# Performance work log

Hardware: AMD Instinct MI355X
Metric: run time of the kernel (lower is better)

Reference implementation:

```python
import jax, jax.numpy as jnp
import numpy as np

B, P, T, H, M = 32, 64, 256, 128, 16
MEAS_E, MOT_E = 64, 64
E = MEAS_E + MOT_E  # total_emb = 128
MAP_SIZE, MAP_EMB = 18, 128
ALPHA = 0.5  # soft-resampling alpha
OUT_DIM = 32 * 9 * 9  # encode output: conv1 stride2 18->9, conv2/3 stride1


def setup_inputs() -> dict:
    key = jax.random.key(0)
    ks = jax.random.split(key, 24)
    def g(i, shape, scale=0.05):
        return jax.random.normal(ks[i], shape, dtype=jnp.float32) * scale
    return {
        "map_in": jax.random.normal(ks[0], (B, 1, MAP_SIZE, MAP_SIZE), dtype=jnp.float32),
        "measurement_in": jax.random.normal(ks[1], (B, T, M), dtype=jnp.float32),
        "motion_in": jax.random.normal(ks[2], (B, T, 3), dtype=jnp.float32),
        "h0": jax.random.uniform(ks[3], (B * P, H), dtype=jnp.float32),
        "eps": jax.random.normal(ks[4], (T, B * P, H), dtype=jnp.float32),
        "u": jax.random.uniform(ks[5], (T, B, P), dtype=jnp.float32),
        "conv1_w": g(6, (16, 1, 5, 5)),
        "conv2_w": g(7, (32, 16, 3, 3)),
        "conv3_w": g(8, (32, 32, 3, 3)),
        "W_mapemb": g(9, (OUT_DIM, MAP_EMB)), "b_mapemb": jnp.zeros((MAP_EMB,), jnp.float32),
        "W_m2meas": g(10, (MAP_EMB, MEAS_E)), "b_m2meas": jnp.zeros((MEAS_E,), jnp.float32),
        "W_m2mot": g(11, (MAP_EMB, MOT_E)), "b_m2mot": jnp.zeros((MOT_E,), jnp.float32),
        "W_meas": g(12, (M, MEAS_E)), "b_meas": jnp.zeros((MEAS_E,), jnp.float32),
        "W_mot": g(13, (3, MOT_E)), "b_mot": jnp.zeros((MOT_E,), jnp.float32),
        "Wz": g(14, (H + E, H)), "bz": jnp.zeros((H,), jnp.float32),
        "Wr": g(15, (H + E, H)), "br": jnp.zeros((H,), jnp.float32),
        "Wn": g(16, (H + E, 2 * H)), "bn": jnp.zeros((2 * H,), jnp.float32),
        "Wo": g(17, (H + E, 1)), "bo": jnp.zeros((1,), jnp.float32),
        "W_label": g(18, (H, 3)), "b_label": jnp.zeros((3,), jnp.float32),
    }


def _encode(map_in, c1, c2, c3):
    # Conv -> ReLU -> BatchNorm(eval: identity w/ default stats) -> Dropout(eval: identity)
    dn = ("NCHW", "OIHW", "NCHW")
    x = jax.lax.conv_general_dilated(map_in, c1, (2, 2), [(2, 2), (2, 2)], dimension_numbers=dn)
    x = jax.nn.relu(x)
    x = jax.lax.conv_general_dilated(x, c2, (1, 1), [(1, 1), (1, 1)], dimension_numbers=dn)
    x = jax.nn.relu(x)
    x = jax.lax.conv_general_dilated(x, c3, (1, 1), [(1, 1), (1, 1)], dimension_numbers=dn)
    return jax.nn.relu(x)


def _pf_forward(map_in, measurement_in, motion_in, h0, eps, u,
                conv1_w, conv2_w, conv3_w,
                W_mapemb, b_mapemb, W_m2meas, b_m2meas, W_m2mot, b_m2mot,
                W_meas, b_meas, W_mot, b_mot,
                Wz, bz, Wr, br, Wn, bn, Wo, bo, W_label, b_label):
    relu = jax.nn.relu
    emb_map = _encode(map_in, conv1_w, conv2_w, conv3_w).reshape(B, -1)
    emb_map = relu(emb_map @ W_mapemb + b_mapemb)
    meas_map = relu(emb_map @ W_m2meas + b_m2meas)           # [B, MEAS_E]
    mot_map = relu(emb_map @ W_m2mot + b_m2mot)              # [B, MOT_E]
    emb_meas = relu(measurement_in @ W_meas + b_meas)        # [B, T, MEAS_E]
    emb_mot = relu(motion_in @ W_mot + b_mot)                # [B, T, MOT_E]
    embedding = jnp.concatenate([emb_meas * meas_map[:, None, :],
                                 emb_mot * mot_map[:, None, :]], axis=2)  # [B,T,E]
    embedding = jnp.tile(embedding, (P, 1, 1))               # [P*B, T, E] (repeat(pNumber,1,1))
    xs_emb = jnp.swapaxes(embedding, 0, 1)                   # [T, P*B, E]
    p0 = jnp.full((B * P, 1), np.log(1.0 / P), dtype=jnp.float32)
    inv_p = (1.0 - ALPHA) / P

    def cell(carry, step):
        h, p = carry                                         # [PB,H], [PB,1]
        x, ep, uu = step                                     # [PB,E], [PB,H], [B,P]
        hx = jnp.concatenate([h, x], axis=1)
        z = jax.nn.sigmoid(hx @ Wz + bz)
        r = jax.nn.sigmoid(hx @ Wr + br)
        n = jnp.concatenate([r * h, x], axis=1) @ Wn + bn
        mu, var = jnp.split(n, 2, axis=1)
        n = mu + ep * jax.nn.softplus(var)                   # reparameterize
        h1 = (1.0 - z) * n + z * h
        lp = jnp.concatenate([h1, x], axis=1) @ Wo + bo + p  # [PB,1] log obs-likelihood + prior
        lp = jax.nn.log_softmax(lp.reshape(P, B), axis=0)    # normalize over particles
        # soft resampling: q = alpha*w + (1-alpha)/P, inverse-CDF multinomial
        w = ALPHA * jnp.exp(lp) + inv_p                      # [P,B], sums to 1 over P
        cdf = jnp.cumsum(w.T, axis=1)                        # [B,P]
        idx = jax.vmap(lambda c, uv: jnp.searchsorted(c, uv * c[-1]))(cdf, uu)
        idx = jnp.clip(idx, 0, P - 1)                        # [B,P]
        idxT = idx.T                                         # [P,B]
        h_new = jnp.take_along_axis(h1.reshape(P, B, H), idxT[:, :, None], axis=0)
        p_g = jnp.take_along_axis(jnp.exp(lp), idxT, axis=0) # [P,B]
        p_new = jnp.log(ALPHA * p_g + inv_p)
        p_new = p_new - jax.scipy.special.logsumexp(p_new, axis=0, keepdims=True)
        h_new = h_new.reshape(B * P, H)
        p_new = p_new.reshape(B * P, 1)
        return (h_new, p_new), (h_new, p_new)

    _, (hs, ps) = jax.lax.scan(cell, (h0, p0), (xs_emb, eps, u))
    # hs: [T, PB, H]; hnn_dropout in eval mode -> identity
    y = jnp.sum(hs.reshape(T, P, B, H) * jnp.exp(ps.reshape(T, P, B, 1)), axis=1)  # [T,B,H]
    y_out = jax.nn.sigmoid(y @ W_label + b_label)            # sigmoid(xy)+sigmoid(h) == sigmoid(all)
    pf_out = jax.nn.sigmoid(hs @ W_label + b_label)          # [T, PB, 3]
    return y_out, pf_out


def reference(map_in, measurement_in, motion_in, h0, eps, u,
              conv1_w, conv2_w, conv3_w,
              W_mapemb, b_mapemb, W_m2meas, b_m2meas, W_m2mot, b_m2mot,
              W_meas, b_meas, W_mot, b_mot,
              Wz, bz, Wr, br, Wn, bn, Wo, bo, W_label, b_label):
    return _pf_forward(map_in, measurement_in, motion_in, h0, eps, u,
                       conv1_w, conv2_w, conv3_w,
                       W_mapemb, b_mapemb, W_m2meas, b_m2meas, W_m2mot, b_m2mot,
                       W_meas, b_meas, W_mot, b_mot,
                       Wz, bz, Wr, br, Wn, bn, Wo, bo, W_label, b_label)
```

## Files before the change

kernel.cpp:

```cpp
#include <hip/hip_runtime.h>
#include <cmath>

namespace {

constexpr int BB = 32, TT = 256, HH = 128;
constexpr int PB = 2048;
constexpr int WGPB = 8;
constexpr double INV_P = 0.0078125;
constexpr float LOG_P0 = -4.1588830833596715f;

__device__ __forceinline__ float sigf(float x) { return 1.f / (1.f + expf(-x)); }

__device__ __forceinline__ float ldc(const float* p) {
  return __hip_atomic_load(p, __ATOMIC_RELAXED, __HIP_MEMORY_SCOPE_AGENT);
}
__device__ __forceinline__ double ldc(const double* p) {
  return __hip_atomic_load(p, __ATOMIC_RELAXED, __HIP_MEMORY_SCOPE_AGENT);
}
__device__ __forceinline__ void stc(unsigned long long* p, unsigned long long v) {
  __hip_atomic_store(p, v, __ATOMIC_RELAXED, __HIP_MEMORY_SCOPE_AGENT);
}
__device__ __forceinline__ void stc(double* p, double v) {
  __hip_atomic_store(p, v, __ATOMIC_RELAXED, __HIP_MEMORY_SCOPE_AGENT);
}

__global__ void pack_kernel(const float* __restrict__ Wz, const float* __restrict__ Wr,
                            const float* __restrict__ Wn,
                            float* __restrict__ WzrH, float* __restrict__ WnH) {
  int tid = blockIdx.x * blockDim.x + threadIdx.x;
  int stride = gridDim.x * blockDim.x;
  for (int i = tid; i < 128 * 256; i += stride) {
    int k = i >> 8, c = i & 255;
    WzrH[i] = (c < 128) ? Wz[k * 128 + c] : Wr[k * 128 + (c - 128)];
    WnH[i] = Wn[k * 256 + c];
  }
}

__global__ __launch_bounds__(256) void encode_kernel(
    const float* __restrict__ map_in, const float* __restrict__ meas_in,
    const float* __restrict__ mot_in,
    const float* __restrict__ c1w, const float* __restrict__ c2w, const float* __restrict__ c3w,
    const float* __restrict__ Wme, const float* __restrict__ bme,
    const float* __restrict__ Wmm, const float* __restrict__ bmm,
    const float* __restrict__ Wmo, const float* __restrict__ bmo,
    const float* __restrict__ Wms, const float* __restrict__ bms,
    const float* __restrict__ Wmt, const float* __restrict__ bmt,
    float* __restrict__ emb) {
  const int b = blockIdx.x;
  const int tid = threadIdx.x;
  __shared__ float ml[324];
  __shared__ float o1[16 * 81];
  __shared__ float o2[32 * 81];
  __shared__ float o3[32 * 81];
  __shared__ float em[128];
  __shared__ float mm[64];
  __shared__ float mo[64];

  for (int i = tid; i < 324; i += 256) ml[i] = map_in[b * 324 + i];
  __syncthreads();
  for (int oid = tid; oid < 16 * 81; oid += 256) {
    int c = oid / 81, r = oid % 81, i = r / 9, j = r % 9;
    float acc = 0.f;
    for (int u = 0; u < 5; ++u) {
      int ii = 2 * i - 2 + u;
      if (ii < 0 || ii >= 18) continue;
      for (int v = 0; v < 5; ++v) {
        int jj = 2 * j - 2 + v;
        if (jj < 0 || jj >= 18) continue;
        acc += ml[ii * 18 + jj] * c1w[c * 25 + u * 5 + v];
      }
    }
    o1[oid] = fmaxf(acc, 0.f);
  }
  __syncthreads();
  for (int oid = tid; oid < 32 * 81; oid += 256) {
    int c = oid / 81, r = oid % 81, i = r / 9, j = r % 9;
    float acc = 0.f;
    for (int ci = 0; ci < 16; ++ci)
      for (int u = 0; u < 3; ++u) {
        int ii = i + u - 1;
        if (ii < 0 || ii >= 9) continue;
        for (int v = 0; v < 3; ++v) {
          int jj = j + v - 1;
          if (jj < 0 || jj >= 9) continue;
          acc += o1[ci * 81 + ii * 9 + jj] * c2w[((c * 16 + ci) * 3 + u) * 3 + v];
        }
      }
    o2[oid] = fmaxf(acc, 0.f);
  }
  __syncthreads();
  for (int oid = tid; oid < 32 * 81; oid += 256) {
    int c = oid / 81, r = oid % 81, i = r / 9, j = r % 9;
    float acc = 0.f;
    for (int ci = 0; ci < 32; ++ci)
      for (int u = 0; u < 3; ++u) {
        int ii = i + u - 1;
        if (ii < 0 || ii >= 9) continue;
        for (int v = 0; v < 3; ++v) {
          int jj = j + v - 1;
          if (jj < 0 || jj >= 9) continue;
          acc += o2[ci * 81 + ii * 9 + jj] * c3w[((c * 32 + ci) * 3 + u) * 3 + v];
        }
      }
    o3[oid] = fmaxf(acc, 0.f);
  }
  __syncthreads();
  if (tid < 128) {
    float acc = 0.f;
    for (int k = 0; k < 2592; ++k) acc += o3[k] * Wme[k * 128 + tid];
    em[tid] = fmaxf(acc + bme[tid], 0.f);
  }
  __syncthreads();
  if (tid < 64) {
    float a1 = 0.f, a2 = 0.f;
    for (int k = 0; k < 128; ++k) {
      a1 += em[k] * Wmm[k * 64 + tid];
      a2 += em[k] * Wmo[k * 64 + tid];
    }
    mm[tid] = fmaxf(a1 + bmm[tid], 0.f);
    mo[tid] = fmaxf(a2 + bmo[tid], 0.f);
  }
  __syncthreads();
  {
    int c = tid & 127;
    for (int t = tid >> 7; t < TT; t += 2) {
      float e;
      if (c < 64) {
        float acc = 0.f;
        for (int m = 0; m < 16; ++m) acc += meas_in[(size_t)(b * TT + t) * 16 + m] * Wms[m * 64 + c];
        e = fmaxf(acc + bms[c], 0.f) * mm[c];
      } else {
        int c2 = c - 64;
        float acc = 0.f;
        for (int m = 0; m < 3; ++m) acc += mot_in[(size_t)(b * TT + t) * 3 + m] * Wmt[m * 64 + c2];
        e = fmaxf(acc + bmt[c2], 0.f) * mo[c2];
      }
      emb[(size_t)(b * TT + t) * 128 + c] = e;
    }
  }
}

__global__ __launch_bounds__(128) void xdot_kernel(
    const float* __restrict__ emb, const float* __restrict__ Wz, const float* __restrict__ Wr,
    const float* __restrict__ Wn, const float* __restrict__ bz, const float* __restrict__ br,
    const float* __restrict__ bn, const float* __restrict__ Wo, const float* __restrict__ bo,
    float* __restrict__ xdot) {
  const int b = blockIdx.y;
  const int t0 = blockIdx.x * 8;
  __shared__ float xl[8][132];
  for (int i = threadIdx.x; i < 8 * 128; i += 128) {
    int r = i >> 7, d = i & 127;
    xl[r][d] = emb[(size_t)(b * TT + t0 + r) * 128 + d];
  }
  __syncthreads();
  const int c = threadIdx.x;
  float az[8] = {0}, ar[8] = {0}, an0[8] = {0}, an1[8] = {0};
  for (int k = 0; k < 128; ++k) {
    float wz = Wz[(128 + k) * 128 + c];
    float wr = Wr[(128 + k) * 128 + c];
    float w0 = Wn[(128 + k) * 256 + c];
    float w1 = Wn[(128 + k) * 256 + 128 + c];
#pragma unroll
    for (int r = 0; r < 8; ++r) {
      float x = xl[r][k];
      az[r] += x * wz; ar[r] += x * wr; an0[r] += x * w0; an1[r] += x * w1;
    }
  }
  for (int r = 0; r < 8; ++r) {
    size_t base = (size_t)((t0 + r) * BB + b) * 516;
    xdot[base + c] = az[r] + bz[c];
    xdot[base + 128 + c] = ar[r] + br[c];
    xdot[base + 256 + c] = an0[r] + bn[c];
    xdot[base + 384 + c] = an1[r] + bn[128 + c];
  }
  if (threadIdx.x < 8) {
    int r = threadIdx.x;
    float acc = 0.f;
    for (int k = 0; k < 128; ++k) acc += xl[r][k] * Wo[128 + k];
    xdot[(size_t)((t0 + r) * BB + b) * 516 + 512] = acc + bo[0];
  }
}

__device__ __forceinline__ void batch_barrier(unsigned* cnt, unsigned target) {
  asm volatile("s_waitcnt vmcnt(0)" ::: "memory");
  __syncthreads();
  if (threadIdx.x == 0) {
    __hip_atomic_fetch_add(cnt, 1u, __ATOMIC_RELAXED, __HIP_MEMORY_SCOPE_AGENT);
    unsigned v;
    do {
      __builtin_amdgcn_s_sleep(1);
      v = __hip_atomic_load(cnt, __ATOMIC_RELAXED, __HIP_MEMORY_SCOPE_AGENT);
    } while (v < target);
  }
  asm volatile("" ::: "memory");
  __syncthreads();
}

__global__ __attribute__((amdgpu_waves_per_eu(2, 2))) __launch_bounds__(512) void scan_kernel(
    const float* __restrict__ h0, const float* __restrict__ eps, const float* __restrict__ u_in,
    const float* __restrict__ Wo, const float* __restrict__ Wlab, const float* __restrict__ blab,
    const float* __restrict__ WzrH, const float* __restrict__ WnH, const float* __restrict__ xdot,
    float* __restrict__ h1buf, double* __restrict__ lpbuf, float* __restrict__ ybuf,
    float* __restrict__ pf_out, unsigned* __restrict__ counters) {
  const int tid = threadIdx.x;
  const int bid = blockIdx.x;
  const int b = bid & 31;
  const int wg = bid >> 5;

  __shared__ float part[8][8][256];
  __shared__ float hl[8][132];
  __shared__ float hT[128][8];
  __shared__ float rhl[8][132];
  __shared__ float rhT[128][8];
  __shared__ float xdl[520];
  __shared__ float wol[128];
  __shared__ float wll[384];
  __shared__ float bll[4];
  __shared__ double cdl[64];
  __shared__ float wnl[64];
  __shared__ int idxl[64];
  __shared__ float pl[8];

  unsigned* cnt = counters + b * 64;

  const int ks = tid >> 6;
  const int l = tid & 63;
  const int d_ = tid & 127;
  const int rp = tid >> 7;

  if (tid < 128) wol[tid] = Wo[tid];
  if (tid >= 128 && tid < 512) wll[tid - 128] = Wlab[tid - 128];
  if (tid < 4) bll[tid] = (tid < 3) ? blab[tid] : 0.f;
  if (tid < 8) pl[tid] = LOG_P0;
  {
    float v0 = h0[(size_t)((8 * wg + 2 * rp) * BB + b) * HH + d_];
    float v1 = h0[(size_t)((8 * wg + 2 * rp + 1) * BB + b) * HH + d_];
    hl[2 * rp][d_] = v0;
    hl[2 * rp + 1][d_] = v1;
    *(float2*)&hT[d_][2 * rp] = make_float2(v0, v1);
  }
  if (tid < 129)
    *(float4*)&xdl[tid * 4] = *(const float4*)&xdot[(size_t)(0 * BB + b) * 516 + tid * 4];

  float4 ep4 = make_float4(0.f, 0.f, 0.f, 0.f);
  if (l < 32)
    ep4 = *(const float4*)&eps[((size_t)0 * PB + (size_t)(8 * wg + ks) * BB + b) * HH + 4 * l];
  __syncthreads();

  for (int t = 0; t < TT; ++t) {
    const int par = t & 1;
    float z0, z1, z2, z3;

    {
      float a[8][4];
#pragma unroll
      for (int r = 0; r < 8; ++r)
#pragma unroll
        for (int j = 0; j < 4; ++j) a[r][j] = 0.f;
      const float* wp = WzrH + (size_t)(16 * ks) * 256 + 4 * l;
#pragma unroll
      for (int kk = 0; kk < 16; ++kk) {
        float4 w4 = *(const float4*)(wp + kk * 256);
        float4 hA = *(const float4*)&hT[16 * ks + kk][0];
        float4 hB = *(const float4*)&hT[16 * ks + kk][4];
        a[0][0] += hA.x * w4.x; a[0][1] += hA.x * w4.y; a[0][2] += hA.x * w4.z; a[0][3] += hA.x * w4.w;
        a[1][0] += hA.y * w4.x; a[1][1] += hA.y * w4.y; a[1][2] += hA.y * w4.z; a[1][3] += hA.y * w4.w;
        a[2][0] += hA.z * w4.x; a[2][1] += hA.z * w4.y; a[2][2] += hA.z * w4.z; a[2][3] += hA.z * w4.w;
        a[3][0] += hA.w * w4.x; a[3][1] += hA.w * w4.y; a[3][2] += hA.w * w4.z; a[3][3] += hA.w * w4.w;
        a[4][0] += hB.x * w4.x; a[4][1] += hB.x * w4.y; a[4][2] += hB.x * w4.z; a[4][3] += hB.x * w4.w;
        a[5][0] += hB.y * w4.x; a[5][1] += hB.y * w4.y; a[5][2] += hB.y * w4.z; a[5][3] += hB.y * w4.w;
        a[6][0] += hB.z * w4.x; a[6][1] += hB.z * w4.y; a[6][2] += hB.z * w4.z; a[6][3] += hB.z * w4.w;
        a[7][0] += hB.w * w4.x; a[7][1] += hB.w * w4.y; a[7][2] += hB.w * w4.z; a[7][3] += hB.w * w4.w;
      }
#pragma unroll
      for (int r = 0; r < 8; ++r)
        *(float4*)&part[ks][r][4 * l] = make_float4(a[r][0], a[r][1], a[r][2], a[r][3]);
    }
    __syncthreads();

    {
      int c0 = 4 * l;
      float s0 = 0.f, s1 = 0.f, s2 = 0.f, s3 = 0.f;
#pragma unroll
      for (int kq = 0; kq < 8; ++kq) {
        float4 p4 = *(const float4*)&part[kq][ks][c0];
        s0 += p4.x; s1 += p4.y; s2 += p4.z; s3 += p4.w;
      }
      s0 = sigf(s0 + xdl[c0 + 0]);
      s1 = sigf(s1 + xdl[c0 + 1]);
      s2 = sigf(s2 + xdl[c0 + 2]);
      s3 = sigf(s3 + xdl[c0 + 3]);
      if (l < 32) {
        z0 = s0; z1 = s1; z2 = s2; z3 = s3;
      } else {
        int cc = c0 - 128;
        float4 rh4;
        rh4.x = s0 * hl[ks][cc + 0];
        rh4.y = s1 * hl[ks][cc + 1];
        rh4.z = s2 * hl[ks][cc + 2];
        rh4.w = s3 * hl[ks][cc + 3];
        *(float4*)&rhl[ks][cc] = rh4;
      }
    }
    __syncthreads();

    {
      float t0v = rhl[2 * rp][d_];
      float t1v = rhl[2 * rp + 1][d_];
      *(float2*)&rhT[d_][2 * rp] = make_float2(t0v, t1v);
    }
    __syncthreads();

    {
      float a[8][4];
#pragma unroll
      for (int r = 0; r < 8; ++r)
#pragma unroll
        for (int j = 0; j < 4; ++j) a[r][j] = 0.f;
      const float* wp = WnH + (size_t)(16 * ks) * 256 + 4 * l;
#pragma unroll
      for (int kk = 0; kk < 16; ++kk) {
        float4 w4 = *(const float4*)(wp + kk * 256);
        float4 hA = *(const float4*)&rhT[16 * ks + kk][0];
        float4 hB = *(const float4*)&rhT[16 * ks + kk][4];
        a[0][0] += hA.x * w4.x; a[0][1] += hA.x * w4.y; a[0][2] += hA.x * w4.z; a[0][3] += hA.x * w4.w;
        a[1][0] += hA.y * w4.x; a[1][1] += hA.y * w4.y; a[1][2] += hA.y * w4.z; a[1][3] += hA.y * w4.w;
        a[2][0] += hA.z * w4.x; a[2][1] += hA.z * w4.y; a[2][2] += hA.z * w4.z; a[2][3] += hA.z * w4.w;
        a[3][0] += hA.w * w4.x; a[3][1] += hA.w * w4.y; a[3][2] += hA.w * w4.z; a[3][3] += hA.w * w4.w;
        a[4][0] += hB.x * w4.x; a[4][1] += hB.x * w4.y; a[4][2] += hB.x * w4.z; a[4][3] += hB.x * w4.w;
        a[5][0] += hB.y * w4.x; a[5][1] += hB.y * w4.y; a[5][2] += hB.y * w4.z; a[5][3] += hB.y * w4.w;
        a[6][0] += hB.z * w4.x; a[6][1] += hB.z * w4.y; a[6][2] += hB.z * w4.z; a[6][3] += hB.z * w4.w;
        a[7][0] += hB.w * w4.x; a[7][1] += hB.w * w4.y; a[7][2] += hB.w * w4.z; a[7][3] += hB.w * w4.w;
      }
#pragma unroll
      for (int r = 0; r < 8; ++r)
        *(float4*)&part[ks][r][4 * l] = make_float4(a[r][0], a[r][1], a[r][2], a[r][3]);
    }
    __syncthreads();

    {
      int c0 = 4 * l;
      float s0 = 0.f, s1 = 0.f, s2 = 0.f, s3 = 0.f;
#pragma unroll
      for (int kq = 0; kq < 8; ++kq) {
        float4 p4 = *(const float4*)&part[kq][ks][c0];
        s0 += p4.x; s1 += p4.y; s2 += p4.z; s3 += p4.w;
      }
      s0 += xdl[256 + c0 + 0];
      s1 += xdl[256 + c0 + 1];
      s2 += xdl[256 + c0 + 2];
      s3 += xdl[256 + c0 + 3];
      float va0 = __shfl(s0, l + 32);
      float va1 = __shfl(s1, l + 32);
      float va2 = __shfl(s2, l + 32);
      float va3 = __shfl(s3, l + 32);
      double lpacc = 0.0;
      if (l < 32) {
        float4 h4 = *(const float4*)&hl[ks][c0];
        float sp0 = fmaxf(va0, 0.f) + log1pf(expf(-fabsf(va0)));
        float sp1 = fmaxf(va1, 0.f) + log1pf(expf(-fabsf(va1)));
        float sp2 = fmaxf(va2, 0.f) + log1pf(expf(-fabsf(va2)));
        float sp3 = fmaxf(va3, 0.f) + log1pf(expf(-fabsf(va3)));
        float h10 = (1.f - z0) * (s0 + ep4.x * sp0) + z0 * h4.x;
        float h11 = (1.f - z1) * (s1 + ep4.y * sp1) + z1 * h4.y;
        float h12 = (1.f - z2) * (s2 + ep4.z * sp2) + z2 * h4.z;
        float h13 = (1.f - z3) * (s3 + ep4.w * sp3) + z3 * h4.w;
        union { unsigned long long u[2]; float f[4]; } pk;
        pk.f[0] = h10; pk.f[1] = h11; pk.f[2] = h12; pk.f[3] = h13;
        unsigned long long* dst = (unsigned long long*)
            &h1buf[((size_t)par * PB + (size_t)(8 * wg + ks) * BB + b) * HH + c0];
        stc(dst + 0, pk.u[0]);
        stc(dst + 1, pk.u[1]);
        lpacc = (double)h10 * (double)wol[c0 + 0] + (double)h11 * (double)wol[c0 + 1] +
                (double)h12 * (double)wol[c0 + 2] + (double)h13 * (double)wol[c0 + 3];
      }
#pragma unroll
      for (int o = 16; o > 0; o >>= 1) lpacc += __shfl_xor(lpacc, o);
      if (l == 0)
        stc(&lpbuf[par * PB + b * 64 + (8 * wg + ks)],
            lpacc + (double)xdl[512] + (double)pl[ks]);
    }

    const int tn = (t + 1 < TT) ? (t + 1) : t;
    float4 xpf = make_float4(0.f, 0.f, 0.f, 0.f);
    if (tid < 129) xpf = *(const float4*)&xdot[(size_t)(tn * BB + b) * 516 + tid * 4];
    if (l < 32)
      ep4 = *(const float4*)&eps[((size_t)tn * PB + (size_t)(8 * wg + ks) * BB + b) * HH + 4 * l];

    batch_barrier(cnt, (unsigned)(WGPB * (t + 1)));

    if (tid < 129) *(float4*)&xdl[tid * 4] = xpf;

    if (ks == 0) {
      double lp = ldc(&lpbuf[par * PB + b * 64 + l]);
      double m = lp;
#pragma unroll
      for (int o = 32; o > 0; o >>= 1) m = fmax(m, __shfl_xor(m, o));
      double e = exp(lp - m);
      double s = e;
#pragma unroll
      for (int o = 32; o > 0; o >>= 1) s += __shfl_xor(s, o);
      double els_v = e / s;
      double w = 0.5 * els_v + INV_P;
      double run = w;
#pragma unroll
      for (int o = 1; o < 64; o <<= 1) {
        double v = __shfl_up(run, o);
        if (l >= o) run += v;
      }
      cdl[l] = run;
      double ctot = __shfl(run, 63);
      double uv = (double)u_in[((size_t)t * BB + b) * 64 + l] * ctot;
      int idx = 0;
#pragma unroll 8
      for (int i = 0; i < 64; ++i) idx += (cdl[i] < uv) ? 1 : 0;
      if (idx > 63) idx = 63;
      idxl[l] = idx;
      double pg = __shfl(els_v, idx);
      double wg_ = 0.5 * pg + INV_P;
      double S2 = wg_;
#pragma unroll
      for (int o = 32; o > 0; o >>= 1) S2 += __shfl_xor(S2, o);
      wnl[l] = (float)(wg_ / S2);
      if ((l >> 3) == wg) pl[l & 7] = (float)(log(wg_) - log(S2));
    }
    __syncthreads();

    {
      int a0i = idxl[8 * wg + 2 * rp];
      int a1i = idxl[8 * wg + 2 * rp + 1];
      float v0 = ldc(&h1buf[((size_t)par * PB + (size_t)a0i * BB + b) * HH + d_]);
      float v1 = ldc(&h1buf[((size_t)par * PB + (size_t)a1i * BB + b) * HH + d_]);
      hl[2 * rp][d_] = v0;
      hl[2 * rp + 1][d_] = v1;
      *(float2*)&hT[d_][2 * rp] = make_float2(v0, v1);
    }
    __syncthreads();

    {
      float ha = hl[ks][l], hb = hl[ks][l + 64];
      float p0 = ha * wll[l * 3 + 0] + hb * wll[(l + 64) * 3 + 0];
      float p1 = ha * wll[l * 3 + 1] + hb * wll[(l + 64) * 3 + 1];
      float p2 = ha * wll[l * 3 + 2] + hb * wll[(l + 64) * 3 + 2];
#pragma unroll
      for (int o = 32; o > 0; o >>= 1) {
        p0 += __shfl_xor(p0, o); p1 += __shfl_xor(p1, o); p2 += __shfl_xor(p2, o);
      }
      if (l == 0) {
        size_t base = ((size_t)t * PB + (size_t)(8 * wg + ks) * BB + b) * 3;
        pf_out[base + 0] = sigf(p0 + bll[0]);
        pf_out[base + 1] = sigf(p1 + bll[1]);
        pf_out[base + 2] = sigf(p2 + bll[2]);
      }
    }

    if (tid < 128) {
      float acc = 0.f;
#pragma unroll
      for (int r = 0; r < 8; ++r) acc += wnl[8 * wg + r] * hl[r][tid];
      atomicAdd(&ybuf[((size_t)t * BB + b) * HH + tid], acc);
    }
  }
}

__global__ __launch_bounds__(256) void yout_kernel(const float* __restrict__ ybuf,
                                                   const float* __restrict__ Wl,
                                                   const float* __restrict__ bl,
                                                   float* __restrict__ out) {
  __shared__ float wls[384];
  __shared__ float bls[3];
  int tid = threadIdx.x;
  for (int i = tid; i < 384; i += 256) wls[i] = Wl[i];
  if (tid < 3) bls[tid] = bl[tid];
  __syncthreads();
  int wv = tid >> 6, ln = tid & 63;
#pragma unroll
  for (int rr = 0; rr < 2; ++rr) {
    int rowi = blockIdx.x * 8 + wv * 2 + rr;
    float ya = ybuf[(size_t)rowi * 128 + ln];
    float yb = ybuf[(size_t)rowi * 128 + ln + 64];
    float p0 = ya * wls[ln * 3 + 0] + yb * wls[(ln + 64) * 3 + 0];
    float p1 = ya * wls[ln * 3 + 1] + yb * wls[(ln + 64) * 3 + 1];
    float p2 = ya * wls[ln * 3 + 2] + yb * wls[(ln + 64) * 3 + 2];
#pragma unroll
    for (int o = 32; o > 0; o >>= 1) {
      p0 += __shfl_xor(p0, o); p1 += __shfl_xor(p1, o); p2 += __shfl_xor(p2, o);
    }
    if (ln == 0) {
      out[(size_t)rowi * 3 + 0] = 1.f / (1.f + expf(-(p0 + bls[0])));
      out[(size_t)rowi * 3 + 1] = 1.f / (1.f + expf(-(p1 + bls[1])));
      out[(size_t)rowi * 3 + 2] = 1.f / (1.f + expf(-(p2 + bls[2])));
    }
  }
}

}

extern "C" void kernel_launch(void* const* d_in, const int* in_sizes, int n_in,
                              void* d_out, int out_size, void* d_ws, size_t ws_size,
                              hipStream_t stream) {
  const float* map_in = (const float*)d_in[0];
  const float* meas_in = (const float*)d_in[1];
  const float* mot_in = (const float*)d_in[2];
  const float* h0 = (const float*)d_in[3];
  const float* eps = (const float*)d_in[4];
  const float* u = (const float*)d_in[5];
  const float* c1w = (const float*)d_in[6];
  const float* c2w = (const float*)d_in[7];
  const float* c3w = (const float*)d_in[8];
  const float* Wme = (const float*)d_in[9];
  const float* bme = (const float*)d_in[10];
  const float* Wmm = (const float*)d_in[11];
  const float* bmm = (const float*)d_in[12];
  const float* Wmo = (const float*)d_in[13];
  const float* bmo = (const float*)d_in[14];
  const float* Wms = (const float*)d_in[15];
  const float* bms = (const float*)d_in[16];
  const float* Wmt = (const float*)d_in[17];
  const float* bmt = (const float*)d_in[18];
  const float* Wz = (const float*)d_in[19];
  const float* bz = (const float*)d_in[20];
  const float* Wr = (const float*)d_in[21];
  const float* br = (const float*)d_in[22];
  const float* Wn = (const float*)d_in[23];
  const float* bn = (const float*)d_in[24];
  const float* Wo = (const float*)d_in[25];
  const float* bo = (const float*)d_in[26];
  const float* Wl = (const float*)d_in[27];
  const float* bl = (const float*)d_in[28];

  char* ws = (char*)d_ws;
  unsigned* counters = (unsigned*)(ws + 0);
  float* WzrH = (float*)(ws + 8192);
  float* WnH = (float*)(ws + 139264);
  float* emb = (float*)(ws + 270336);
  float* xdot = (float*)(ws + 4464640);
  float* h1buf = (float*)(ws + 21372928);
  double* lpbuf = (double*)(ws + 23470080);
  float* ybuf = (float*)(ws + 23502848);
  if (ws_size < 27697152) return;

  float* out = (float*)d_out;
  float* pf_out = out + 24576;

  hipMemsetAsync(counters, 0, 8192, stream);
  hipMemsetAsync(ybuf, 0, 4194304, stream);
  hipLaunchKernelGGL(pack_kernel, dim3(128), dim3(256), 0, stream, Wz, Wr, Wn, WzrH, WnH);
  hipLaunchKernelGGL(encode_kernel, dim3(32), dim3(256), 0, stream, map_in, meas_in, mot_in,
                     c1w, c2w, c3w, Wme, bme, Wmm, bmm, Wmo, bmo, Wms, bms, Wmt, bmt, emb);
  hipLaunchKernelGGL(xdot_kernel, dim3(32, 32), dim3(128), 0, stream, emb, Wz, Wr, Wn, bz, br,
                     bn, Wo, bo, xdot);
  hipLaunchKernelGGL(scan_kernel, dim3(256), dim3(512), 0, stream, h0, eps, u, Wo, Wl, bl,
                     WzrH, WnH, xdot, h1buf, lpbuf, ybuf, pf_out, counters);
  hipLaunchKernelGGL(yout_kernel, dim3(1024), dim3(256), 0, stream, ybuf, Wl, bl, out);
}
```

Measured before the change: 5.288 ms.

## Precompute z/r gate matmul on un-resampled particles before resampling

Resampling only permutes particle rows, so the per-step z/r gate projection (h·Wzr) is now computed on each workgroup's own new hidden states right after the GRU update. It is published to a global zr buffer, and after resampling each particle gathers its row by ancestor index. This moves the gate matmul off the critical path that follows the resampling barrier. A second counter/barrier lets it overlap with the wait for log-weights. The cost is an extra global buffer (aliasing the emb workspace), another cross-workgroup barrier per step, and pf/y outputs shifted one step later with an epilogue.

```diff
diff --git a/kernel.cpp b/kernel.cpp
--- a/kernel.cpp
+++ b/kernel.cpp
@@ -17,10 +17,16 @@
 __device__ __forceinline__ double ldc(const double* p) {
   return __hip_atomic_load(p, __ATOMIC_RELAXED, __HIP_MEMORY_SCOPE_AGENT);
 }
+__device__ __forceinline__ unsigned long long ldc(const unsigned long long* p) {
+  return __hip_atomic_load(p, __ATOMIC_RELAXED, __HIP_MEMORY_SCOPE_AGENT);
+}
 __device__ __forceinline__ void stc(unsigned long long* p, unsigned long long v) {
   __hip_atomic_store(p, v, __ATOMIC_RELAXED, __HIP_MEMORY_SCOPE_AGENT);
 }
 __device__ __forceinline__ void stc(double* p, double v) {
+  __hip_atomic_store(p, v, __ATOMIC_RELAXED, __HIP_MEMORY_SCOPE_AGENT);
+}
+__device__ __forceinline__ void stc(float* p, float v) {
   __hip_atomic_store(p, v, __ATOMIC_RELAXED, __HIP_MEMORY_SCOPE_AGENT);
 }
 
@@ -181,27 +187,12 @@
   }
 }
 
-__device__ __forceinline__ void batch_barrier(unsigned* cnt, unsigned target) {
-  asm volatile("s_waitcnt vmcnt(0)" ::: "memory");
-  __syncthreads();
-  if (threadIdx.x == 0) {
-    __hip_atomic_fetch_add(cnt, 1u, __ATOMIC_RELAXED, __HIP_MEMORY_SCOPE_AGENT);
-    unsigned v;
-    do {
-      __builtin_amdgcn_s_sleep(1);
-      v = __hip_atomic_load(cnt, __ATOMIC_RELAXED, __HIP_MEMORY_SCOPE_AGENT);
-    } while (v < target);
-  }
-  asm volatile("" ::: "memory");
-  __syncthreads();
-}
-
 __global__ __attribute__((amdgpu_waves_per_eu(2, 2))) __launch_bounds__(512) void scan_kernel(
     const float* __restrict__ h0, const float* __restrict__ eps, const float* __restrict__ u_in,
     const float* __restrict__ Wo, const float* __restrict__ Wlab, const float* __restrict__ blab,
     const float* __restrict__ WzrH, const float* __restrict__ WnH, const float* __restrict__ xdot,
-    float* __restrict__ h1buf, double* __restrict__ lpbuf, float* __restrict__ ybuf,
-    float* __restrict__ pf_out, unsigned* __restrict__ counters) {
+    float* __restrict__ h1buf, double* __restrict__ lpbuf, float* __restrict__ zrbuf,
+    float* __restrict__ ybuf, float* __restrict__ pf_out, unsigned* __restrict__ counters) {
   const int tid = threadIdx.x;
   const int bid = blockIdx.x;
   const int b = bid & 31;
@@ -209,9 +200,10 @@
 
   __shared__ float part[8][8][256];
   __shared__ float hl[8][132];
-  __shared__ float hT[128][8];
   __shared__ float rhl[8][132];
   __shared__ float rhT[128][8];
+  __shared__ float h1l[8][132];
+  __shared__ float h1T[128][8];
   __shared__ float xdl[520];
   __shared__ float wol[128];
   __shared__ float wll[384];
@@ -221,7 +213,8 @@
   __shared__ int idxl[64];
   __shared__ float pl[8];
 
-  unsigned* cnt = counters + b * 64;
+  unsigned* cnt1 = counters + b * 32;
+  unsigned* cnt2 = counters + 1024 + b * 32;
 
   const int ks = tid >> 6;
   const int l = tid & 63;
@@ -232,64 +225,134 @@
   if (tid >= 128 && tid < 512) wll[tid - 128] = Wlab[tid - 128];
   if (tid < 4) bll[tid] = (tid < 3) ? blab[tid] : 0.f;
   if (tid < 8) pl[tid] = LOG_P0;
+  if (tid < 64) idxl[tid] = tid;
+
   {
     float v0 = h0[(size_t)((8 * wg + 2 * rp) * BB + b) * HH + d_];
     float v1 = h0[(size_t)((8 * wg + 2 * rp + 1) * BB + b) * HH + d_];
-    hl[2 * rp][d_] = v0;
-    hl[2 * rp + 1][d_] = v1;
-    *(float2*)&hT[d_][2 * rp] = make_float2(v0, v1);
-  }
-  if (tid < 129)
-    *(float4*)&xdl[tid * 4] = *(const float4*)&xdot[(size_t)(0 * BB + b) * 516 + tid * 4];
-
+    h1l[2 * rp][d_] = v0;
+    h1l[2 * rp + 1][d_] = v1;
+    stc(&h1buf[((size_t)1 * PB + (size_t)(8 * wg + 2 * rp) * BB + b) * HH + d_], v0);
+    stc(&h1buf[((size_t)1 * PB + (size_t)(8 * wg + 2 * rp + 1) * BB + b) * HH + d_], v1);
+  }
+  __syncthreads();
+  {
+    float t0v = h1l[2 * rp][d_];
+    float t1v = h1l[2 * rp + 1][d_];
+    *(float2*)&h1T[d_][2 * rp] = make_float2(t0v, t1v);
+  }
+  __syncthreads();
+  {
+    float a[8][4];
+#pragma unroll
+    for (int r = 0; r < 8; ++r)
+#pragma unroll
+      for (int j = 0; j < 4; ++j) a[r][j] = 0.f;
+    const float* wp = WzrH + (size_t)(16 * ks) * 256 + 4 * l;
+#pragma unroll
+    for (int kk = 0; kk < 16; ++kk) {
+      float4 w4 = *(const float4*)(wp + kk * 256);
+      float4 hA = *(const float4*)&h1T[16 * ks + kk][0];
+      float4 hB = *(const float4*)&h1T[16 * ks + kk][4];
+      a[0][0] += hA.x * w4.x; a[0][1] += hA.x * w4.y; a[0][2] += hA.x * w4.z; a[0][3] += hA.x * w4.w;
+      a[1][0] += hA.y * w4.x; a[1][1] += hA.y * w4.y; a[1][2] += hA.y * w4.z; a[1][3] += hA.y * w4.w;
+      a[2][0] += hA.z * w4.x; a[2][1] += hA.z * w4.y; a[2][2] += hA.z * w4.z; a[2][3] += hA.z * w4.w;
+      a[3][0] += hA.w * w4.x; a[3][1] += hA.w * w4.y; a[3][2] += hA.w * w4.z; a[3][3] += hA.w * w4.w;
+      a[4][0] += hB.x * w4.x; a[4][1] += hB.x * w4.y; a[4][2] += hB.x * w4.z; a[4][3] += hB.x * w4.w;
+      a[5][0] += hB.y * w4.x; a[5][1] += hB.y * w4.y; a[5][2] += hB.y * w4.z; a[5][3] += hB.y * w4.w;
+      a[6][0] += hB.z * w4.x; a[6][1] += hB.z * w4.y; a[6][2] += hB.z * w4.z; a[6][3] += hB.z * w4.w;
+      a[7][0] += hB.w * w4.x; a[7][1] += hB.w * w4.y; a[7][2] += hB.w * w4.z; a[7][3] += hB.w * w4.w;
+    }
+#pragma unroll
+    for (int r = 0; r < 8; ++r)
+      *(float4*)&part[ks][r][4 * l] = make_float4(a[r][0], a[r][1], a[r][2], a[r][3]);
+  }
+  __syncthreads();
+  {
+    int c0 = 4 * l;
+    float s0 = 0.f, s1 = 0.f, s2 = 0.f, s3 = 0.f;
+#pragma unroll
+    for (int kq = 0; kq < 8; ++kq) {
+      float4 p4 = *(const float4*)&part[kq][ks][c0];
+      s0 += p4.x; s1 += p4.y; s2 += p4.z; s3 += p4.w;
+    }
+    union { unsigned long long u[2]; float f[4]; } pk;
+    pk.f[0] = s0; pk.f[1] = s1; pk.f[2] = s2; pk.f[3] = s3;
+    unsigned long long* dst = (unsigned long long*)
+        &zrbuf[(size_t)0 * (PB * 256) + (size_t)(b * 64 + 8 * wg + ks) * 256 + c0];
+    stc(dst + 0, pk.u[0]);
+    stc(dst + 1, pk.u[1]);
+  }
+  asm volatile("s_waitcnt vmcnt(0)" ::: "memory");
+  __syncthreads();
+  if (tid == 0) __hip_atomic_fetch_add(cnt2, 1u, __ATOMIC_RELAXED, __HIP_MEMORY_SCOPE_AGENT);
+  if (tid == 0) {
+    unsigned v;
+    do {
+      __builtin_amdgcn_s_sleep(1);
+      v = __hip_atomic_load(cnt2, __ATOMIC_RELAXED, __HIP_MEMORY_SCOPE_AGENT);
+    } while (v < (unsigned)WGPB);
+  }
+  asm volatile("" ::: "memory");
+  __syncthreads();
+
+  float4 xpf = make_float4(0.f, 0.f, 0.f, 0.f);
+  if (tid < 129) xpf = *(const float4*)&xdot[(size_t)(0 * BB + b) * 516 + tid * 4];
   float4 ep4 = make_float4(0.f, 0.f, 0.f, 0.f);
   if (l < 32)
     ep4 = *(const float4*)&eps[((size_t)0 * PB + (size_t)(8 * wg + ks) * BB + b) * HH + 4 * l];
-  __syncthreads();
 
   for (int t = 0; t < TT; ++t) {
     const int par = t & 1;
     float z0, z1, z2, z3;
 
     {
-      float a[8][4];
-#pragma unroll
-      for (int r = 0; r < 8; ++r)
-#pragma unroll
-        for (int j = 0; j < 4; ++j) a[r][j] = 0.f;
-      const float* wp = WzrH + (size_t)(16 * ks) * 256 + 4 * l;
-#pragma unroll
-      for (int kk = 0; kk < 16; ++kk) {
-        float4 w4 = *(const float4*)(wp + kk * 256);
-        float4 hA = *(const float4*)&hT[16 * ks + kk][0];
-        float4 hB = *(const float4*)&hT[16 * ks + kk][4];
-        a[0][0] += hA.x * w4.x; a[0][1] += hA.x * w4.y; a[0][2] += hA.x * w4.z; a[0][3] += hA.x * w4.w;
-        a[1][0] += hA.y * w4.x; a[1][1] += hA.y * w4.y; a[1][2] += hA.y * w4.z; a[1][3] += hA.y * w4.w;
-        a[2][0] += hA.z * w4.x; a[2][1] += hA.z * w4.y; a[2][2] += hA.z * w4.z; a[2][3] += hA.z * w4.w;
-        a[3][0] += hA.w * w4.x; a[3][1] += hA.w * w4.y; a[3][2] += hA.w * w4.z; a[3][3] += hA.w * w4.w;
-        a[4][0] += hB.x * w4.x; a[4][1] += hB.x * w4.y; a[4][2] += hB.x * w4.z; a[4][3] += hB.x * w4.w;
-        a[5][0] += hB.y * w4.x; a[5][1] += hB.y * w4.y; a[5][2] += hB.y * w4.z; a[5][3] += hB.y * w4.w;
-        a[6][0] += hB.z * w4.x; a[6][1] += hB.z * w4.y; a[6][2] += hB.z * w4.z; a[6][3] += hB.z * w4.w;
-        a[7][0] += hB.w * w4.x; a[7][1] += hB.w * w4.y; a[7][2] += hB.w * w4.z; a[7][3] += hB.w * w4.w;
-      }
-#pragma unroll
-      for (int r = 0; r < 8; ++r)
-        *(float4*)&part[ks][r][4 * l] = make_float4(a[r][0], a[r][1], a[r][2], a[r][3]);
-    }
-    __syncthreads();
+      int a0i = idxl[8 * wg + 2 * rp];
+      int a1i = idxl[8 * wg + 2 * rp + 1];
+      float v0 = ldc(&h1buf[((size_t)(par ^ 1) * PB + (size_t)a0i * BB + b) * HH + d_]);
+      float v1 = ldc(&h1buf[((size_t)(par ^ 1) * PB + (size_t)a1i * BB + b) * HH + d_]);
+      hl[2 * rp][d_] = v0;
+      hl[2 * rp + 1][d_] = v1;
+    }
+    if (tid < 129) *(float4*)&xdl[tid * 4] = xpf;
+    float uval = 0.f;
+    if (ks == 0) uval = u_in[((size_t)t * BB + b) * 64 + l];
+    __syncthreads();
+    if (t > 0) {
+      float ha = hl[ks][l], hb = hl[ks][l + 64];
+      float p0 = ha * wll[l * 3 + 0] + hb * wll[(l + 64) * 3 + 0];
+      float p1 = ha * wll[l * 3 + 1] + hb * wll[(l + 64) * 3 + 1];
+      float p2 = ha * wll[l * 3 + 2] + hb * wll[(l + 64) * 3 + 2];
+#pragma unroll
+      for (int o = 32; o > 0; o >>= 1) {
+        p0 += __shfl_xor(p0, o); p1 += __shfl_xor(p1, o); p2 += __shfl_xor(p2, o);
+      }
+      if (l == 0) {
+        size_t base = ((size_t)(t - 1) * PB + (size_t)(8 * wg + ks) * BB + b) * 3;
+        pf_out[base + 0] = sigf(p0 + bll[0]);
+        pf_out[base + 1] = sigf(p1 + bll[1]);
+        pf_out[base + 2] = sigf(p2 + bll[2]);
+      }
+      if (tid < 128) {
+        float acc = 0.f;
+#pragma unroll
+        for (int r = 0; r < 8; ++r) acc += wnl[8 * wg + r] * hl[r][tid];
+        atomicAdd(&ybuf[((size_t)(t - 1) * BB + b) * HH + tid], acc);
+      }
+    }
 
     {
+      int row = b * 64 + idxl[8 * wg + ks];
+      const unsigned long long* zsrc = (const unsigned long long*)
+          &zrbuf[(size_t)par * (PB * 256) + (size_t)row * 256 + 4 * l];
+      unsigned long long q0 = ldc(zsrc + 0), q1 = ldc(zsrc + 1);
+      union { unsigned long long u[2]; float f[4]; } pk;
+      pk.u[0] = q0; pk.u[1] = q1;
       int c0 = 4 * l;
-      float s0 = 0.f, s1 = 0.f, s2 = 0.f, s3 = 0.f;
-#pragma unroll
-      for (int kq = 0; kq < 8; ++kq) {
-        float4 p4 = *(const float4*)&part[kq][ks][c0];
-        s0 += p4.x; s1 += p4.y; s2 += p4.z; s3 += p4.w;
-      }
-      s0 = sigf(s0 + xdl[c0 + 0]);
-      s1 = sigf(s1 + xdl[c0 + 1]);
-      s2 = sigf(s2 + xdl[c0 + 2]);
-      s3 = sigf(s3 + xdl[c0 + 3]);
+      float s0 = sigf(pk.f[0] + xdl[c0 + 0]);
+      float s1 = sigf(pk.f[1] + xdl[c0 + 1]);
+      float s2 = sigf(pk.f[2] + xdl[c0 + 2]);
+      float s3 = sigf(pk.f[3] + xdl[c0 + 3]);
       if (l < 32) {
         z0 = s0; z1 = s1; z2 = s2; z3 = s3;
       } else {
@@ -303,7 +366,6 @@
       }
     }
     __syncthreads();
-
     {
       float t0v = rhl[2 * rp][d_];
       float t1v = rhl[2 * rp + 1][d_];
@@ -365,6 +427,7 @@
         float h11 = (1.f - z1) * (s1 + ep4.y * sp1) + z1 * h4.y;
         float h12 = (1.f - z2) * (s2 + ep4.z * sp2) + z2 * h4.z;
         float h13 = (1.f - z3) * (s3 + ep4.w * sp3) + z3 * h4.w;
+        *(float4*)&h1l[ks][c0] = make_float4(h10, h11, h12, h13);
         union { unsigned long long u[2]; float f[4]; } pk;
         pk.f[0] = h10; pk.f[1] = h11; pk.f[2] = h12; pk.f[3] = h13;
         unsigned long long* dst = (unsigned long long*)
@@ -380,16 +443,77 @@
         stc(&lpbuf[par * PB + b * 64 + (8 * wg + ks)],
             lpacc + (double)xdl[512] + (double)pl[ks]);
     }
-
+    asm volatile("s_waitcnt vmcnt(0)" ::: "memory");
+    __syncthreads();
+    if (tid == 0)
+      __hip_atomic_fetch_add(cnt1, 1u, __ATOMIC_RELAXED, __HIP_MEMORY_SCOPE_AGENT);
+    {
+      float t0v = h1l[2 * rp][d_];
+      float t1v = h1l[2 * rp + 1][d_];
+      *(float2*)&h1T[d_][2 * rp] = make_float2(t0v, t1v);
+    }
+    __syncthreads();
+
+    if (t < TT - 1) {
+      float a[8][4];
+#pragma unroll
+      for (int r = 0; r < 8; ++r)
+#pragma unroll
+        for (int j = 0; j < 4; ++j) a[r][j] = 0.f;
+      const float* wp = WzrH + (size_t)(16 * ks) * 256 + 4 * l;
+#pragma unroll
+      for (int kk = 0; kk < 16; ++kk) {
+        float4 w4 = *(const float4*)(wp + kk * 256);
+        float4 hA = *(const float4*)&h1T[16 * ks + kk][0];
+        float4 hB = *(const float4*)&h1T[16 * ks + kk][4];
+        a[0][0] += hA.x * w4.x; a[0][1] += hA.x * w4.y; a[0][2] += hA.x * w4.z; a[0][3] += hA.x * w4.w;
+        a[1][0] += hA.y * w4.x; a[1][1] += hA.y * w4.y; a[1][2] += hA.y * w4.z; a[1][3] += hA.y * w4.w;
+        a[2][0] += hA.z * w4.x; a[2][1] += hA.z * w4.y; a[2][2] += hA.z * w4.z; a[2][3] += hA.z * w4.w;
+        a[3][0] += hA.w * w4.x; a[3][1] += hA.w * w4.y; a[3][2] += hA.w * w4.z; a[3][3] += hA.w * w4.w;
+        a[4][0] += hB.x * w4.x; a[4][1] += hB.x * w4.y; a[4][2] += hB.x * w4.z; a[4][3] += hB.x * w4.w;
+        a[5][0] += hB.y * w4.x; a[5][1] += hB.y * w4.y; a[5][2] += hB.y * w4.z; a[5][3] += hB.y * w4.w;
+        a[6][0] += hB.z * w4.x; a[6][1] += hB.z * w4.y; a[6][2] += hB.z * w4.z; a[6][3] += hB.z * w4.w;
+        a[7][0] += hB.w * w4.x; a[7][1] += hB.w * w4.y; a[7][2] += hB.w * w4.z; a[7][3] += hB.w * w4.w;
+      }
+#pragma unroll
+      for (int r = 0; r < 8; ++r)
+        *(float4*)&part[ks][r][4 * l] = make_float4(a[r][0], a[r][1], a[r][2], a[r][3]);
+      __syncthreads();
+      {
+        int c0 = 4 * l;
+        float s0 = 0.f, s1 = 0.f, s2 = 0.f, s3 = 0.f;
+#pragma unroll
+        for (int kq = 0; kq < 8; ++kq) {
+          float4 p4 = *(const float4*)&part[kq][ks][c0];
+          s0 += p4.x; s1 += p4.y; s2 += p4.z; s3 += p4.w;
+        }
+        union { unsigned long long u[2]; float f[4]; } pk;
+        pk.f[0] = s0; pk.f[1] = s1; pk.f[2] = s2; pk.f[3] = s3;
+        unsigned long long* dst = (unsigned long long*)
+            &zrbuf[(size_t)(par ^ 1) * (PB * 256) + (size_t)(b * 64 + 8 * wg + ks) * 256 + c0];
+        stc(dst + 0, pk.u[0]);
+        stc(dst + 1, pk.u[1]);
+      }
+    }
     const int tn = (t + 1 < TT) ? (t + 1) : t;
-    float4 xpf = make_float4(0.f, 0.f, 0.f, 0.f);
+    xpf = make_float4(0.f, 0.f, 0.f, 0.f);
     if (tid < 129) xpf = *(const float4*)&xdot[(size_t)(tn * BB + b) * 516 + tid * 4];
     if (l < 32)
       ep4 = *(const float4*)&eps[((size_t)tn * PB + (size_t)(8 * wg + ks) * BB + b) * HH + 4 * l];
-
-    batch_barrier(cnt, (unsigned)(WGPB * (t + 1)));
-
-    if (tid < 129) *(float4*)&xdl[tid * 4] = xpf;
+    asm volatile("s_waitcnt vmcnt(0)" ::: "memory");
+    __syncthreads();
+    if (tid == 0 && t < TT - 1)
+      __hip_atomic_fetch_add(cnt2, 1u, __ATOMIC_RELAXED, __HIP_MEMORY_SCOPE_AGENT);
+
+    if (tid == 0) {
+      unsigned v;
+      do {
+        __builtin_amdgcn_s_sleep(1);
+        v = __hip_atomic_load(cnt1, __ATOMIC_RELAXED, __HIP_MEMORY_SCOPE_AGENT);
+      } while (v < (unsigned)(WGPB * (t + 1)));
+    }
+    asm volatile("" ::: "memory");
+    __syncthreads();
 
     if (ks == 0) {
       double lp = ldc(&lpbuf[par * PB + b * 64 + l]);
@@ -410,7 +534,7 @@
       }
       cdl[l] = run;
       double ctot = __shfl(run, 63);
-      double uv = (double)u_in[((size_t)t * BB + b) * 64 + l] * ctot;
+      double uv = (double)uval * ctot;
       int idx = 0;
 #pragma unroll 8
       for (int i = 0; i < 64; ++i) idx += (cdl[i] < uv) ? 1 : 0;
@@ -426,39 +550,49 @@
     }
     __syncthreads();
 
-    {
-      int a0i = idxl[8 * wg + 2 * rp];
-      int a1i = idxl[8 * wg + 2 * rp + 1];
-      float v0 = ldc(&h1buf[((size_t)par * PB + (size_t)a0i * BB + b) * HH + d_]);
-      float v1 = ldc(&h1buf[((size_t)par * PB + (size_t)a1i * BB + b) * HH + d_]);
-      hl[2 * rp][d_] = v0;
-      hl[2 * rp + 1][d_] = v1;
-      *(float2*)&hT[d_][2 * rp] = make_float2(v0, v1);
-    }
-    __syncthreads();
-
-    {
-      float ha = hl[ks][l], hb = hl[ks][l + 64];
-      float p0 = ha * wll[l * 3 + 0] + hb * wll[(l + 64) * 3 + 0];
-      float p1 = ha * wll[l * 3 + 1] + hb * wll[(l + 64) * 3 + 1];
-      float p2 = ha * wll[l * 3 + 2] + hb * wll[(l + 64) * 3 + 2];
-#pragma unroll
-      for (int o = 32; o > 0; o >>= 1) {
-        p0 += __shfl_xor(p0, o); p1 += __shfl_xor(p1, o); p2 += __shfl_xor(p2, o);
-      }
-      if (l == 0) {
-        size_t base = ((size_t)t * PB + (size_t)(8 * wg + ks) * BB + b) * 3;
-        pf_out[base + 0] = sigf(p0 + bll[0]);
-        pf_out[base + 1] = sigf(p1 + bll[1]);
-        pf_out[base + 2] = sigf(p2 + bll[2]);
-      }
-    }
-
+    if (t < TT - 1) {
+      if (tid == 0) {
+        unsigned v;
+        do {
+          __builtin_amdgcn_s_sleep(1);
+          v = __hip_atomic_load(cnt2, __ATOMIC_RELAXED, __HIP_MEMORY_SCOPE_AGENT);
+        } while (v < (unsigned)(WGPB * (t + 2)));
+      }
+      asm volatile("" ::: "memory");
+      __syncthreads();
+    }
+  }
+
+  {
+    const int par = TT & 1;
+    int a0i = idxl[8 * wg + 2 * rp];
+    int a1i = idxl[8 * wg + 2 * rp + 1];
+    float v0 = ldc(&h1buf[((size_t)(par ^ 1) * PB + (size_t)a0i * BB + b) * HH + d_]);
+    float v1 = ldc(&h1buf[((size_t)(par ^ 1) * PB + (size_t)a1i * BB + b) * HH + d_]);
+    hl[2 * rp][d_] = v0;
+    hl[2 * rp + 1][d_] = v1;
+  }
+  __syncthreads();
+  {
+    float ha = hl[ks][l], hb = hl[ks][l + 64];
+    float p0 = ha * wll[l * 3 + 0] + hb * wll[(l + 64) * 3 + 0];
+    float p1 = ha * wll[l * 3 + 1] + hb * wll[(l + 64) * 3 + 1];
+    float p2 = ha * wll[l * 3 + 2] + hb * wll[(l + 64) * 3 + 2];
+#pragma unroll
+    for (int o = 32; o > 0; o >>= 1) {
+      p0 += __shfl_xor(p0, o); p1 += __shfl_xor(p1, o); p2 += __shfl_xor(p2, o);
+    }
+    if (l == 0) {
+      size_t base = ((size_t)(TT - 1) * PB + (size_t)(8 * wg + ks) * BB + b) * 3;
+      pf_out[base + 0] = sigf(p0 + bll[0]);
+      pf_out[base + 1] = sigf(p1 + bll[1]);
+      pf_out[base + 2] = sigf(p2 + bll[2]);
+    }
     if (tid < 128) {
       float acc = 0.f;
 #pragma unroll
       for (int r = 0; r < 8; ++r) acc += wnl[8 * wg + r] * hl[r][tid];
-      atomicAdd(&ybuf[((size_t)t * BB + b) * HH + tid], acc);
+      atomicAdd(&ybuf[((size_t)(TT - 1) * BB + b) * HH + tid], acc);
     }
   }
 }
@@ -539,6 +673,7 @@
   double* lpbuf = (double*)(ws + 23470080);
   float* ybuf = (float*)(ws + 23502848);
   if (ws_size < 27697152) return;
+  float* zrbuf = emb;
 
   float* out = (float*)d_out;
   float* pf_out = out + 24576;
@@ -551,6 +686,6 @@
   hipLaunchKernelGGL(xdot_kernel, dim3(32, 32), dim3(128), 0, stream, emb, Wz, Wr, Wn, bz, br,
                      bn, Wo, bo, xdot);
   hipLaunchKernelGGL(scan_kernel, dim3(256), dim3(512), 0, stream, h0, eps, u, Wo, Wl, bl,
-                     WzrH, WnH, xdot, h1buf, lpbuf, ybuf, pf_out, counters);
+                     WzrH, WnH, xdot, h1buf, lpbuf, zrbuf, ybuf, pf_out, counters);
   hipLaunchKernelGGL(yout_kernel, dim3(1024), dim3(256), 0, stream, ybuf, Wl, bl, out);
 }
```

New measurement: 6.195 ms. 17.2% more time.

## Compute resampling redundantly per wave with shuffles, dropping block-wide syncs

Applied to the files above, without the earlier changes.

Instead of having only thread 0 spin on the per-batch counter and wave 0 compute the resampling indices and weights through shared memory, every wave now polls the counter itself. Each wave then recomputes the softmax, CDF and index search redundantly using cross-lane shuffles. This removes one __syncthreads and the LDS round trips in every timestep, and the u value is now loaded before the barrier. In exchange, all waves poll the global counter, which adds memory traffic, and every wave does the 64-entry double-precision resampling math.

```diff
diff --git a/kernel.cpp b/kernel.cpp
--- a/kernel.cpp
+++ b/kernel.cpp
@@ -181,21 +181,6 @@
   }
 }
 
-__device__ __forceinline__ void batch_barrier(unsigned* cnt, unsigned target) {
-  asm volatile("s_waitcnt vmcnt(0)" ::: "memory");
-  __syncthreads();
-  if (threadIdx.x == 0) {
-    __hip_atomic_fetch_add(cnt, 1u, __ATOMIC_RELAXED, __HIP_MEMORY_SCOPE_AGENT);
-    unsigned v;
-    do {
-      __builtin_amdgcn_s_sleep(1);
-      v = __hip_atomic_load(cnt, __ATOMIC_RELAXED, __HIP_MEMORY_SCOPE_AGENT);
-    } while (v < target);
-  }
-  asm volatile("" ::: "memory");
-  __syncthreads();
-}
-
 __global__ __attribute__((amdgpu_waves_per_eu(2, 2))) __launch_bounds__(512) void scan_kernel(
     const float* __restrict__ h0, const float* __restrict__ eps, const float* __restrict__ u_in,
     const float* __restrict__ Wo, const float* __restrict__ Wlab, const float* __restrict__ blab,
@@ -216,10 +201,6 @@
   __shared__ float wol[128];
   __shared__ float wll[384];
   __shared__ float bll[4];
-  __shared__ double cdl[64];
-  __shared__ float wnl[64];
-  __shared__ int idxl[64];
-  __shared__ float pl[8];
 
   unsigned* cnt = counters + b * 64;
 
@@ -231,7 +212,9 @@
   if (tid < 128) wol[tid] = Wo[tid];
   if (tid >= 128 && tid < 512) wll[tid - 128] = Wlab[tid - 128];
   if (tid < 4) bll[tid] = (tid < 3) ? blab[tid] : 0.f;
-  if (tid < 8) pl[tid] = LOG_P0;
+  float pl_mine = LOG_P0;
+  int myidx = l;
+  float mywn = 0.f;
   {
     float v0 = h0[(size_t)((8 * wg + 2 * rp) * BB + b) * HH + d_];
     float v1 = h0[(size_t)((8 * wg + 2 * rp + 1) * BB + b) * HH + d_];
@@ -378,7 +361,7 @@
       for (int o = 16; o > 0; o >>= 1) lpacc += __shfl_xor(lpacc, o);
       if (l == 0)
         stc(&lpbuf[par * PB + b * 64 + (8 * wg + ks)],
-            lpacc + (double)xdl[512] + (double)pl[ks]);
+            lpacc + (double)xdl[512] + (double)pl_mine);
     }
 
     const int tn = (t + 1 < TT) ? (t + 1) : t;
@@ -386,12 +369,26 @@
     if (tid < 129) xpf = *(const float4*)&xdot[(size_t)(tn * BB + b) * 516 + tid * 4];
     if (l < 32)
       ep4 = *(const float4*)&eps[((size_t)tn * PB + (size_t)(8 * wg + ks) * BB + b) * HH + 4 * l];
-
-    batch_barrier(cnt, (unsigned)(WGPB * (t + 1)));
+    float uval = u_in[((size_t)t * BB + b) * 64 + l];
+
+    asm volatile("s_waitcnt vmcnt(0)" ::: "memory");
+    __syncthreads();
+    if (tid == 0)
+      __hip_atomic_fetch_add(cnt, 1u, __ATOMIC_RELAXED, __HIP_MEMORY_SCOPE_AGENT);
 
     if (tid < 129) *(float4*)&xdl[tid * 4] = xpf;
 
-    if (ks == 0) {
+    {
+      const unsigned tgt = (unsigned)(WGPB * (t + 1));
+      unsigned v;
+      do {
+        __builtin_amdgcn_s_sleep(1);
+        v = __hip_atomic_load(cnt, __ATOMIC_RELAXED, __HIP_MEMORY_SCOPE_AGENT);
+      } while (v < tgt);
+    }
+    asm volatile("" ::: "memory");
+
+    {
       double lp = ldc(&lpbuf[par * PB + b * 64 + l]);
       double m = lp;
 #pragma unroll
@@ -408,27 +405,29 @@
         double v = __shfl_up(run, o);
         if (l >= o) run += v;
       }
-      cdl[l] = run;
       double ctot = __shfl(run, 63);
-      double uv = (double)u_in[((size_t)t * BB + b) * 64 + l] * ctot;
+      double uv = (double)uval * ctot;
       int idx = 0;
 #pragma unroll 8
-      for (int i = 0; i < 64; ++i) idx += (cdl[i] < uv) ? 1 : 0;
+      for (int i = 0; i < 64; ++i) {
+        double ci = __shfl(run, i);
+        idx += (ci < uv) ? 1 : 0;
+      }
       if (idx > 63) idx = 63;
-      idxl[l] = idx;
+      myidx = idx;
       double pg = __shfl(els_v, idx);
       double wg_ = 0.5 * pg + INV_P;
       double S2 = wg_;
 #pragma unroll
       for (int o = 32; o > 0; o >>= 1) S2 += __shfl_xor(S2, o);
-      wnl[l] = (float)(wg_ / S2);
-      if ((l >> 3) == wg) pl[l & 7] = (float)(log(wg_) - log(S2));
-    }
-    __syncthreads();
-
-    {
-      int a0i = idxl[8 * wg + 2 * rp];
-      int a1i = idxl[8 * wg + 2 * rp + 1];
+      mywn = (float)(wg_ / S2);
+      float pn_l = (float)(log(wg_) - log(S2));
+      pl_mine = __shfl(pn_l, 8 * wg + ks);
+    }
+
+    {
+      int a0i = __shfl(myidx, 8 * wg + 2 * rp);
+      int a1i = __shfl(myidx, 8 * wg + 2 * rp + 1);
       float v0 = ldc(&h1buf[((size_t)par * PB + (size_t)a0i * BB + b) * HH + d_]);
       float v1 = ldc(&h1buf[((size_t)par * PB + (size_t)a1i * BB + b) * HH + d_]);
       hl[2 * rp][d_] = v0;
@@ -457,7 +456,7 @@
     if (tid < 128) {
       float acc = 0.f;
 #pragma unroll
-      for (int r = 0; r < 8; ++r) acc += wnl[8 * wg + r] * hl[r][tid];
+      for (int r = 0; r < 8; ++r) acc += __shfl(mywn, 8 * wg + r) * hl[r][tid];
       atomicAdd(&ybuf[((size_t)t * BB + b) * HH + tid], acc);
     }
   }
```

After: 6.626 ms. +25.3%, slower.
